# Performance work log

Hardware: AMD Instinct MI355X
Metric: run time of the kernel (lower is better)

## Reference

```python
import jax, jax.numpy as jnp
import numpy as np

EPS = 1e-5  # torch BatchNorm2d default


def _conv5x5(x, w, b):
    # x: [N,1,H,W], w: [1,1,5,5], b: [1]; stride 1, padding 2 (SAME)
    out = jax.lax.conv_general_dilated(
        x, w, window_strides=(1, 1), padding=((2, 2), (2, 2)),
        dimension_numbers=("NCHW", "OIHW", "NCHW"))
    return out + b[None, :, None, None]


def _batchnorm(x, gamma, beta):
    # training-mode BatchNorm2d: per-channel batch stats over (N,H,W), biased var
    mean = jnp.mean(x, axis=(0, 2, 3), keepdims=True)
    var = jnp.mean(jnp.square(x - mean), axis=(0, 2, 3), keepdims=True)
    xhat = (x - mean) * jax.lax.rsqrt(var + EPS)
    return xhat * gamma[None, :, None, None] + beta[None, :, None, None]


def _shrinkage(x, lumdb):
    return x + 0.5 * (jnp.sqrt(jnp.square(x - lumdb) + 1.0)
                      - jnp.sqrt(jnp.square(x + lumdb) + 1.0))


def setup_inputs() -> dict:
    key = jax.random.key(0)
    k1, k2, k3 = jax.random.split(key, 3)
    y = jax.random.normal(k1, (64, 1, 512, 512), dtype=jnp.float32)
    # kaiming-uniform-ish init for a 1x1x5x5 conv
    fan_in = 25.0
    bound = 1.0 / np.sqrt(fan_in)
    conv_w = jax.random.uniform(k2, (1, 1, 5, 5), jnp.float32, -bound, bound)
    conv_b = jax.random.uniform(k3, (1,), jnp.float32, -bound, bound)
    gamma = jnp.ones((1,), jnp.float32)
    beta = jnp.zeros((1,), jnp.float32)
    lambd = jnp.array([2.0, 1.0, 0.0], jnp.float32)
    return {"y": y, "conv_w": conv_w, "conv_b": conv_b,
            "gamma": gamma, "beta": beta, "lambd": lambd}


def reference(y, conv_w, conv_b, gamma, beta, lambd):
    x_k = y
    # unrolled LISTA iteration 1
    x = _batchnorm(_conv5x5(x_k, conv_w, conv_b), gamma, beta)
    x = _shrinkage(x, lambd[0])
    o12 = _batchnorm(_conv5x5(x, conv_w, conv_b), gamma, beta)
    x = _batchnorm(_conv5x5(x_k, conv_w, conv_b), gamma, beta)
    # iteration 2
    x = _shrinkage(o12 + x, lambd[1])
    o22 = _batchnorm(_conv5x5(x, conv_w, conv_b), gamma, beta)
    x = _batchnorm(_conv5x5(x_k, conv_w, conv_b), gamma, beta)
    # iteration 3
    x = _shrinkage(o22 + x, lambd[2])
    return x
```

## Files before the change

kernel.cpp:

```cpp
#include <hip/hip_runtime.h>
#include <math.h>

#define HH 512
#define WW 512
#define NTOT (64u*512u*512u)
#define NBLK 1024
#define TS 128
#define TROWS 132
#define TCH 18
#define TPIT 152
#define NTASK (TROWS*TCH)
#define NITER 10

typedef __attribute__((ext_vector_type(8))) short short8;
typedef __attribute__((ext_vector_type(4))) float f32x4;

__device__ __forceinline__ float fsqrtf(float x) { return __builtin_amdgcn_sqrtf(x); }

__device__ __forceinline__ float shrinkf(float x, float l) {
    float a = x - l, b = x + l;
    return x + 0.5f * (fsqrtf(__builtin_fmaf(a, a, 1.f)) - fsqrtf(__builtin_fmaf(b, b, 1.f)));
}

__device__ __forceinline__ float bf2f(unsigned int u) {
    union { unsigned int i; float f; } cv;
    cv.i = u << 16;
    return cv.f;
}
__device__ __forceinline__ float lo2f(unsigned int p) {
    union { unsigned int i; float f; } cv; cv.i = p << 16; return cv.f;
}
__device__ __forceinline__ float hi2f(unsigned int p) {
    union { unsigned int i; float f; } cv; cv.i = p & 0xffff0000u; return cv.f;
}

__device__ __forceinline__ unsigned int cvtpk(float lo, float hi) {
    unsigned int r;
    asm("v_cvt_pk_bf16_f32 %0, %1, %2" : "=v"(r) : "v"(lo), "v"(hi));
    return r;
}

__device__ __forceinline__ void bf8(uint4 u, float* f) {
    f[0] = bf2f(u.x & 0xffffu); f[1] = bf2f(u.x >> 16);
    f[2] = bf2f(u.y & 0xffffu); f[3] = bf2f(u.y >> 16);
    f[4] = bf2f(u.z & 0xffffu); f[5] = bf2f(u.z >> 16);
    f[6] = bf2f(u.w & 0xffffu); f[7] = bf2f(u.w >> 16);
}

template <int MODE, bool OBF>
__global__ __launch_bounds__(256, 4) void conv_k(
    const float* __restrict__ yin,
    const unsigned short* __restrict__ t1,
    const unsigned short* __restrict__ t2,
    unsigned short* __restrict__ outbf,
    float* __restrict__ outf32,
    const float* __restrict__ wgt,
    const float* __restrict__ bias,
    const float* __restrict__ stats,
    const float* __restrict__ lambd,
    float* __restrict__ partials)
{
    __shared__ unsigned short tile[TROWS * TPIT];

    const int tid = threadIdx.x;
    const int by = blockIdx.y * TS;
    const int bx = blockIdx.x * TS;
    const size_t ibase = (size_t)blockIdx.z * (HH * WW);

    float s1 = 0.f, h1 = 0.f, s2v = 0.f, h2 = 0.f, lam = 0.f;
    if constexpr (MODE == 1) { s1 = stats[0]; h1 = stats[1]; lam = lambd[0]; }
    if constexpr (MODE == 2) {
        s1 = stats[0]; h1 = stats[1]; s2v = stats[2]; h2 = stats[3]; lam = lambd[1];
    }

    float wloc[25];
#pragma unroll
    for (int i = 0; i < 25; i++) wloc[i] = wgt[i];

    const int lane = tid & 63;
    const int lm = lane & 15;
    const int kb = lane >> 4;
    const int basei = kb * 8 - lm - 6;
    short8 bfr[5];
#pragma unroll
    for (int ky = 0; ky < 5; ky++) {
        unsigned pkw[4];
#pragma unroll
        for (int jj = 0; jj < 4; jj++) {
            float v0 = 0.f, v1 = 0.f;
            const int i0 = basei + 2 * jj, i1 = i0 + 1;
#pragma unroll
            for (int t = 0; t < 5; t++) {
                if (i0 == t) v0 = wloc[ky * 5 + t];
                if (i1 == t) v1 = wloc[ky * 5 + t];
            }
            pkw[jj] = cvtpk(v0, v1);
        }
        union { unsigned u[4]; short8 s; } cv;
        cv.u[0] = pkw[0]; cv.u[1] = pkw[1]; cv.u[2] = pkw[2]; cv.u[3] = pkw[3];
        bfr[ky] = cv.s;
    }

    uint4 curA = make_uint4(0u,0u,0u,0u), curB = make_uint4(0u,0u,0u,0u);
    {
        const int task = tid;
        const int row = task / TCH;
        const int ch  = task - row * TCH;
        const int gy  = by + row - 2;
        const int gx0 = bx + ch * 8 - 8;
        if (gy >= 0 && gy < HH && gx0 >= 0 && gx0 <= WW - 8) {
            const size_t g = ibase + (size_t)gy * WW + gx0;
            if constexpr (MODE == 0) {
                curA = *(const uint4*)(yin + g);
                curB = *(const uint4*)(yin + g + 4);
            } else if constexpr (MODE == 1) {
                curA = *(const uint4*)(t1 + g);
            } else {
                curA = *(const uint4*)(t1 + g);
                curB = *(const uint4*)(t2 + g);
            }
        }
    }
#pragma unroll
    for (int t = 0; t < NITER; t++) {
        uint4 nxtA = make_uint4(0u,0u,0u,0u), nxtB = make_uint4(0u,0u,0u,0u);
        if (t + 1 < NITER) {
            const int ntsk = tid + (t + 1) * 256;
            const int row = ntsk / TCH;
            const int ch  = ntsk - row * TCH;
            const int gy  = by + row - 2;
            const int gx0 = bx + ch * 8 - 8;
            if (ntsk < NTASK && gy >= 0 && gy < HH && gx0 >= 0 && gx0 <= WW - 8) {
                const size_t g = ibase + (size_t)gy * WW + gx0;
                if constexpr (MODE == 0) {
                    nxtA = *(const uint4*)(yin + g);
                    nxtB = *(const uint4*)(yin + g + 4);
                } else if constexpr (MODE == 1) {
                    nxtA = *(const uint4*)(t1 + g);
                } else {
                    nxtA = *(const uint4*)(t1 + g);
                    nxtB = *(const uint4*)(t2 + g);
                }
            }
        }
        const int task = tid + t * 256;
        if (task < NTASK) {
            const int row = task / TCH;
            const int ch  = task - row * TCH;
            uint4 pk = make_uint4(0u,0u,0u,0u);
            if constexpr (MODE == 0) {
                const float4 a = *(const float4*)&curA;
                const float4 b = *(const float4*)&curB;
                pk.x = cvtpk(a.x, a.y); pk.y = cvtpk(a.z, a.w);
                pk.z = cvtpk(b.x, b.y); pk.w = cvtpk(b.z, b.w);
            } else if constexpr (MODE == 1) {
                float f1[8]; bf8(curA, f1);
                float v[8];
#pragma unroll
                for (int k = 0; k < 8; k++)
                    v[k] = shrinkf(__builtin_fmaf(f1[k], s1, h1), lam);
                pk.x = cvtpk(v[0], v[1]); pk.y = cvtpk(v[2], v[3]);
                pk.z = cvtpk(v[4], v[5]); pk.w = cvtpk(v[6], v[7]);
            } else {
                float f1[8], f2[8]; bf8(curA, f1); bf8(curB, f2);
                float v[8];
#pragma unroll
                for (int k = 0; k < 8; k++) {
                    float x = __builtin_fmaf(f2[k], s2v, h2)
                            + __builtin_fmaf(f1[k], s1, h1);
                    v[k] = shrinkf(x, lam);
                }
                pk.x = cvtpk(v[0], v[1]); pk.y = cvtpk(v[2], v[3]);
                pk.z = cvtpk(v[4], v[5]); pk.w = cvtpk(v[6], v[7]);
            }
            const int gy  = by + row - 2;
            const int gx0 = bx + ch * 8 - 8;
            if (!(gy >= 0 && gy < HH && gx0 >= 0 && gx0 <= WW - 8))
                pk = make_uint4(0u,0u,0u,0u);
            *(uint4*)&tile[row * TPIT + ch * 8] = pk;
        }
        curA = nxtA; curB = nxtB;
    }

    const float b0 = bias[0];
    __syncthreads();

    const int wv = tid >> 6;
    const int r0w = wv * 32;

    f32x4 acc[2][8];
#pragma unroll
    for (int st = 0; st < 2; st++)
#pragma unroll
        for (int ct = 0; ct < 8; ct++)
            acc[st][ct] = (f32x4){0.f, 0.f, 0.f, 0.f};

#pragma unroll
    for (int ky = 0; ky < 5; ky++) {
        const short8 b = bfr[ky];
#pragma unroll
        for (int st = 0; st < 2; st++) {
            const unsigned short* ab = &tile[(r0w + st * 16 + lm + ky) * TPIT + kb * 8];
#pragma unroll
            for (int ct = 0; ct < 8; ct++) {
                short8 a = *(const short8*)(ab + ct * 16);
                acc[st][ct] = __builtin_amdgcn_mfma_f32_16x16x32_bf16(a, b, acc[st][ct], 0, 0, 0);
            }
        }
    }

    float s = 0.f, q = 0.f;
#pragma unroll
    for (int st = 0; st < 2; st++) {
#pragma unroll
        for (int ct = 0; ct < 8; ct++) {
            const f32x4 a = acc[st][ct];
            const int grow0 = by + r0w + st * 16 + kb * 4;
            const size_t base = ibase + (size_t)grow0 * WW + bx + ct * 16 + lm;
            if constexpr (OBF) {
                unsigned p01 = cvtpk(a[0] + b0, a[1] + b0);
                unsigned p23 = cvtpk(a[2] + b0, a[3] + b0);
                outbf[base]          = (unsigned short)(p01 & 0xffffu);
                outbf[base + WW]     = (unsigned short)(p01 >> 16);
                outbf[base + 2 * WW] = (unsigned short)(p23 & 0xffffu);
                outbf[base + 3 * WW] = (unsigned short)(p23 >> 16);
                float fr0 = lo2f(p01), fr1 = hi2f(p01), fr2 = lo2f(p23), fr3 = hi2f(p23);
                s += fr0 + fr1 + fr2 + fr3;
                q = __builtin_fmaf(fr0, fr0, __builtin_fmaf(fr1, fr1,
                    __builtin_fmaf(fr2, fr2, __builtin_fmaf(fr3, fr3, q))));
            } else {
                float f0 = a[0] + b0, f1v = a[1] + b0, f2v = a[2] + b0, f3v = a[3] + b0;
                outf32[base]          = f0;
                outf32[base + WW]     = f1v;
                outf32[base + 2 * WW] = f2v;
                outf32[base + 3 * WW] = f3v;
                s += f0 + f1v + f2v + f3v;
                q = __builtin_fmaf(f0, f0, __builtin_fmaf(f1v, f1v,
                    __builtin_fmaf(f2v, f2v, __builtin_fmaf(f3v, f3v, q))));
            }
        }
    }

    __syncthreads();
    float* red = (float*)tile;
    red[tid] = s; red[256 + tid] = q;
    __syncthreads();
    for (int off = 128; off > 0; off >>= 1) {
        if (tid < off) { red[tid] += red[tid + off]; red[256 + tid] += red[256 + tid + off]; }
        __syncthreads();
    }
    if (tid == 0) {
        const int bid = (blockIdx.z * 4 + blockIdx.y) * 4 + blockIdx.x;
        partials[bid * 2] = red[0];
        partials[bid * 2 + 1] = red[256];
    }
}

__global__ __launch_bounds__(256) void finalize_k(
    const float* __restrict__ partials, float* __restrict__ stats, int stage,
    const float* __restrict__ gamma, const float* __restrict__ beta)
{
    __shared__ double rs[256], rq[256];
    const int tid = threadIdx.x;
    double s = 0.0, q = 0.0;
    for (int i = tid; i < NBLK; i += 256) { s += partials[2 * i]; q += partials[2 * i + 1]; }
    rs[tid] = s; rq[tid] = q;
    __syncthreads();
    for (int off = 128; off > 0; off >>= 1) {
        if (tid < off) { rs[tid] += rs[tid + off]; rq[tid] += rq[tid + off]; }
        __syncthreads();
    }
    if (tid == 0) {
        double mean = rs[0] / (double)NTOT;
        double var = rq[0] / (double)NTOT - mean * mean;
        double scl = (double)gamma[0] / sqrt(var + 1e-5);
        stats[2 * stage] = (float)scl;
        stats[2 * stage + 1] = (float)((double)beta[0] - mean * scl);
    }
}

template <bool T3BF>
__global__ __launch_bounds__(256) void final_k(
    const unsigned short* __restrict__ t1,
    const unsigned short* __restrict__ t3b,
    float* __restrict__ io,
    const float* __restrict__ stats, const float* __restrict__ lambd)
{
    const float s1 = stats[0], h1 = stats[1], s3 = stats[4], h3 = stats[5];
    const float lam = lambd[2];
    const size_t base = ((size_t)blockIdx.x * 256 + threadIdx.x) * 8;

    uint4 u1 = *(const uint4*)(t1 + base);
    float f1[8]; bf8(u1, f1);

    float t3v[8];
    if constexpr (T3BF) {
        uint4 u3 = *(const uint4*)(t3b + base);
        bf8(u3, t3v);
    } else {
        float4 a0 = *(const float4*)(io + base);
        float4 a1 = *(const float4*)(io + base + 4);
        t3v[0]=a0.x; t3v[1]=a0.y; t3v[2]=a0.z; t3v[3]=a0.w;
        t3v[4]=a1.x; t3v[5]=a1.y; t3v[6]=a1.z; t3v[7]=a1.w;
    }

    float r[8];
#pragma unroll
    for (int k = 0; k < 8; k++) {
        float v = __builtin_fmaf(t3v[k], s3, h3) + __builtin_fmaf(f1[k], s1, h1);
        r[k] = shrinkf(v, lam);
    }
    *(float4*)(io + base)     = make_float4(r[0], r[1], r[2], r[3]);
    *(float4*)(io + base + 4) = make_float4(r[4], r[5], r[6], r[7]);
}

extern "C" void kernel_launch(void* const* d_in, const int* in_sizes, int n_in,
                              void* d_out, int out_size, void* d_ws, size_t ws_size,
                              hipStream_t stream)
{
    const float* y     = (const float*)d_in[0];
    const float* wgt   = (const float*)d_in[1];
    const float* bias  = (const float*)d_in[2];
    const float* gamma = (const float*)d_in[3];
    const float* beta  = (const float*)d_in[4];
    const float* lambd = (const float*)d_in[5];
    float* out = (float*)d_out;

    char* ws = (char*)d_ws;
    unsigned short* t1 = (unsigned short*)ws;
    unsigned short* t2 = (unsigned short*)(ws + 33554432ull);
    unsigned short* t3 = (unsigned short*)(ws + 67108864ull);
    const bool t3bf = (ws_size >= 100696088ull);
    const size_t poff = t3bf ? 100663296ull : 67108864ull;
    float* partials = (float*)(ws + poff);
    float* stats    = (float*)(ws + poff + 32768ull);

    dim3 grid(4, 4, 64), blk(256);
    conv_k<0, true><<<grid, blk, 0, stream>>>(y, nullptr, nullptr, t1, nullptr,
                                              wgt, bias, stats, lambd, partials);
    finalize_k<<<1, blk, 0, stream>>>(partials, stats, 0, gamma, beta);
    conv_k<1, true><<<grid, blk, 0, stream>>>(nullptr, t1, nullptr, t2, nullptr,
                                              wgt, bias, stats, lambd, partials);
    finalize_k<<<1, blk, 0, stream>>>(partials, stats, 1, gamma, beta);
    if (t3bf) {
        conv_k<2, true><<<grid, blk, 0, stream>>>(nullptr, t1, t2, t3, nullptr,
                                                  wgt, bias, stats, lambd, partials);
        finalize_k<<<1, blk, 0, stream>>>(partials, stats, 2, gamma, beta);
        final_k<true><<<8192, blk, 0, stream>>>(t1, t3, out, stats, lambd);
    } else {
        conv_k<2, false><<<grid, blk, 0, stream>>>(nullptr, t1, t2, nullptr, out,
                                                   wgt, bias, stats, lambd, partials);
        finalize_k<<<1, blk, 0, stream>>>(partials, stats, 2, gamma, beta);
        final_k<false><<<8192, blk, 0, stream>>>(t1, nullptr, out, stats, lambd);
    }
}
```

Measured before the change: 108.6 us.

## Stage bf16 conv inputs into LDS with direct global-to-LDS loads

For the two bf16-input modes, the register-prefetch staging loop is replaced by `global_load_lds` calls. These copy the raw tiles straight into shared memory (a second buffer holds the second input in mode 2). The BN-affine plus shrinkage transform then runs in place on the LDS tile before the MFMA convolution. This aims to cut register pressure and VGPR round-trips during loading, but it drops the row padding (pitch 144 instead of 152), which may add LDS bank conflicts in the MFMA reads. Mode 2 also doubles its LDS footprint and lowers its occupancy hint to 2.

```diff
diff --git a/kernel.cpp b/kernel.cpp
--- a/kernel.cpp
+++ b/kernel.cpp
@@ -8,8 +8,8 @@
 #define TS 128
 #define TROWS 132
 #define TCH 18
-#define TPIT 152
 #define NTASK (TROWS*TCH)
+#define NTASKP 2432
 #define NITER 10
 
 typedef __attribute__((ext_vector_type(8))) short short8;
@@ -47,8 +47,15 @@
     f[6] = bf2f(u.w & 0xffffu); f[7] = bf2f(u.w >> 16);
 }
 
+__device__ __forceinline__ void gload16(const unsigned short* g, unsigned short* l) {
+    __builtin_amdgcn_global_load_lds(
+        (const __attribute__((address_space(1))) void*)g,
+        (__attribute__((address_space(3))) void*)l,
+        16, 0, 0);
+}
+
 template <int MODE, bool OBF>
-__global__ __launch_bounds__(256, 4) void conv_k(
+__global__ __launch_bounds__(256, (MODE == 2 ? 2 : 4)) void conv_k(
     const float* __restrict__ yin,
     const unsigned short* __restrict__ t1,
     const unsigned short* __restrict__ t2,
@@ -60,7 +67,10 @@
     const float* __restrict__ lambd,
     float* __restrict__ partials)
 {
-    __shared__ unsigned short tile[TROWS * TPIT];
+    constexpr int TP_ = (MODE == 0) ? 152 : 144;
+    constexpr int TILE_SH = (MODE == 0) ? (TROWS * 152) : (NTASKP * 8);
+    __shared__ unsigned short tile[TILE_SH];
+    __shared__ unsigned short raw2[(MODE == 2) ? NTASKP * 8 : 8];
 
     const int tid = threadIdx.x;
     const int by = blockIdx.y * TS;
@@ -101,85 +111,107 @@
         bfr[ky] = cv.s;
     }
 
-    uint4 curA = make_uint4(0u,0u,0u,0u), curB = make_uint4(0u,0u,0u,0u);
-    {
-        const int task = tid;
-        const int row = task / TCH;
-        const int ch  = task - row * TCH;
-        const int gy  = by + row - 2;
-        const int gx0 = bx + ch * 8 - 8;
-        if (gy >= 0 && gy < HH && gx0 >= 0 && gx0 <= WW - 8) {
-            const size_t g = ibase + (size_t)gy * WW + gx0;
-            if constexpr (MODE == 0) {
+    if constexpr (MODE == 0) {
+        uint4 curA = make_uint4(0u,0u,0u,0u), curB = make_uint4(0u,0u,0u,0u);
+        {
+            const int task = tid;
+            const int row = task / TCH;
+            const int ch  = task - row * TCH;
+            const int gy  = by + row - 2;
+            const int gx0 = bx + ch * 8 - 8;
+            if (gy >= 0 && gy < HH && gx0 >= 0 && gx0 <= WW - 8) {
+                const size_t g = ibase + (size_t)gy * WW + gx0;
                 curA = *(const uint4*)(yin + g);
                 curB = *(const uint4*)(yin + g + 4);
-            } else if constexpr (MODE == 1) {
-                curA = *(const uint4*)(t1 + g);
-            } else {
-                curA = *(const uint4*)(t1 + g);
-                curB = *(const uint4*)(t2 + g);
-            }
-        }
-    }
-#pragma unroll
-    for (int t = 0; t < NITER; t++) {
-        uint4 nxtA = make_uint4(0u,0u,0u,0u), nxtB = make_uint4(0u,0u,0u,0u);
-        if (t + 1 < NITER) {
-            const int ntsk = tid + (t + 1) * 256;
-            const int row = ntsk / TCH;
-            const int ch  = ntsk - row * TCH;
-            const int gy  = by + row - 2;
-            const int gx0 = bx + ch * 8 - 8;
-            if (ntsk < NTASK && gy >= 0 && gy < HH && gx0 >= 0 && gx0 <= WW - 8) {
-                const size_t g = ibase + (size_t)gy * WW + gx0;
-                if constexpr (MODE == 0) {
+            }
+        }
+#pragma unroll
+        for (int t = 0; t < NITER; t++) {
+            uint4 nxtA = make_uint4(0u,0u,0u,0u), nxtB = make_uint4(0u,0u,0u,0u);
+            if (t + 1 < NITER) {
+                const int ntsk = tid + (t + 1) * 256;
+                const int row = ntsk / TCH;
+                const int ch  = ntsk - row * TCH;
+                const int gy  = by + row - 2;
+                const int gx0 = bx + ch * 8 - 8;
+                if (ntsk < NTASK && gy >= 0 && gy < HH && gx0 >= 0 && gx0 <= WW - 8) {
+                    const size_t g = ibase + (size_t)gy * WW + gx0;
                     nxtA = *(const uint4*)(yin + g);
                     nxtB = *(const uint4*)(yin + g + 4);
-                } else if constexpr (MODE == 1) {
-                    nxtA = *(const uint4*)(t1 + g);
-                } else {
-                    nxtA = *(const uint4*)(t1 + g);
-                    nxtB = *(const uint4*)(t2 + g);
                 }
             }
-        }
-        const int task = tid + t * 256;
-        if (task < NTASK) {
-            const int row = task / TCH;
-            const int ch  = task - row * TCH;
-            uint4 pk = make_uint4(0u,0u,0u,0u);
-            if constexpr (MODE == 0) {
+            const int task = tid + t * 256;
+            if (task < NTASK) {
+                const int row = task / TCH;
+                const int ch  = task - row * TCH;
+                uint4 pk = make_uint4(0u,0u,0u,0u);
                 const float4 a = *(const float4*)&curA;
                 const float4 b = *(const float4*)&curB;
                 pk.x = cvtpk(a.x, a.y); pk.y = cvtpk(a.z, a.w);
                 pk.z = cvtpk(b.x, b.y); pk.w = cvtpk(b.z, b.w);
-            } else if constexpr (MODE == 1) {
-                float f1[8]; bf8(curA, f1);
-                float v[8];
-#pragma unroll
-                for (int k = 0; k < 8; k++)
-                    v[k] = shrinkf(__builtin_fmaf(f1[k], s1, h1), lam);
-                pk.x = cvtpk(v[0], v[1]); pk.y = cvtpk(v[2], v[3]);
-                pk.z = cvtpk(v[4], v[5]); pk.w = cvtpk(v[6], v[7]);
-            } else {
-                float f1[8], f2[8]; bf8(curA, f1); bf8(curB, f2);
-                float v[8];
-#pragma unroll
-                for (int k = 0; k < 8; k++) {
-                    float x = __builtin_fmaf(f2[k], s2v, h2)
-                            + __builtin_fmaf(f1[k], s1, h1);
-                    v[k] = shrinkf(x, lam);
+                const int gy  = by + row - 2;
+                const int gx0 = bx + ch * 8 - 8;
+                if (!(gy >= 0 && gy < HH && gx0 >= 0 && gx0 <= WW - 8))
+                    pk = make_uint4(0u,0u,0u,0u);
+                *(uint4*)&tile[row * TP_ + ch * 8] = pk;
+            }
+            curA = nxtA; curB = nxtB;
+        }
+    } else {
+        const int wv4 = tid >> 6;
+#pragma unroll
+        for (int r = 0; r < NITER; r++) {
+            const int task0 = r * 256 + wv4 * 64;
+            if (task0 < NTASK) {
+                const int task = task0 + lane;
+                const int row = task / TCH;
+                const int ch  = task - row * TCH;
+                const int gy  = by + row - 2;
+                const int gx0 = bx + ch * 8 - 8;
+                const bool ok = (task < NTASK) && gy >= 0 && gy < HH &&
+                                gx0 >= 0 && gx0 <= WW - 8;
+                const size_t g = ok ? (ibase + (size_t)gy * WW + gx0) : ibase;
+                gload16(t1 + g, &tile[task * 8]);
+                if constexpr (MODE == 2)
+                    gload16(t2 + g, &raw2[task * 8]);
+            }
+        }
+        __syncthreads();
+
+#pragma unroll
+        for (int t = 0; t < NITER; t++) {
+            const int task = tid + t * 256;
+            if (task < NTASK) {
+                const int row = task / TCH;
+                const int ch  = task - row * TCH;
+                const int gy  = by + row - 2;
+                const int gx0 = bx + ch * 8 - 8;
+                const bool ok = gy >= 0 && gy < HH && gx0 >= 0 && gx0 <= WW - 8;
+                uint4 pk = make_uint4(0u,0u,0u,0u);
+                if (ok) {
+                    uint4 u1 = *(const uint4*)&tile[task * 8];
+                    float f1[8]; bf8(u1, f1);
+                    float v[8];
+                    if constexpr (MODE == 1) {
+#pragma unroll
+                        for (int k = 0; k < 8; k++)
+                            v[k] = shrinkf(__builtin_fmaf(f1[k], s1, h1), lam);
+                    } else {
+                        uint4 u2 = *(const uint4*)&raw2[task * 8];
+                        float f2[8]; bf8(u2, f2);
+#pragma unroll
+                        for (int k = 0; k < 8; k++) {
+                            float x = __builtin_fmaf(f2[k], s2v, h2)
+                                    + __builtin_fmaf(f1[k], s1, h1);
+                            v[k] = shrinkf(x, lam);
+                        }
+                    }
+                    pk.x = cvtpk(v[0], v[1]); pk.y = cvtpk(v[2], v[3]);
+                    pk.z = cvtpk(v[4], v[5]); pk.w = cvtpk(v[6], v[7]);
                 }
-                pk.x = cvtpk(v[0], v[1]); pk.y = cvtpk(v[2], v[3]);
-                pk.z = cvtpk(v[4], v[5]); pk.w = cvtpk(v[6], v[7]);
-            }
-            const int gy  = by + row - 2;
-            const int gx0 = bx + ch * 8 - 8;
-            if (!(gy >= 0 && gy < HH && gx0 >= 0 && gx0 <= WW - 8))
-                pk = make_uint4(0u,0u,0u,0u);
-            *(uint4*)&tile[row * TPIT + ch * 8] = pk;
-        }
-        curA = nxtA; curB = nxtB;
+                *(uint4*)&tile[task * 8] = pk;
+            }
+        }
     }
 
     const float b0 = bias[0];
@@ -200,7 +232,7 @@
         const short8 b = bfr[ky];
 #pragma unroll
         for (int st = 0; st < 2; st++) {
-            const unsigned short* ab = &tile[(r0w + st * 16 + lm + ky) * TPIT + kb * 8];
+            const unsigned short* ab = &tile[(r0w + st * 16 + lm + ky) * TP_ + kb * 8];
 #pragma unroll
             for (int ct = 0; ct < 8; ct++) {
                 short8 a = *(const short8*)(ab + ct * 16);
```

New measurement: 115.5 us. +6.3%, slower.
